# Kernel tuning notes

Hardware: AMD Instinct MI355X
Metric: run time of the kernel (lower is better)

The kernel has to match this reference:

```python
import jax, jax.numpy as jnp
import numpy as np

B, M, T, D, V = 16, 4096, 4, 256, 40000
HOPS, NLAYER, CONV_MAX = 3, 3, 512
PAD = 1  # PAD_token: embedding row zeroed (padding_idx)


def setup_inputs() -> dict:
    key = jax.random.key(0)
    ks = jax.random.split(key, 10)
    story = jax.random.randint(ks[0], (B, M, T), 0, V)
    conv_len = jax.random.randint(ks[1], (B,), 1, CONV_MAX)
    kb_len = jax.random.randint(ks[2], (B,), 0, M - CONV_MAX)
    query = jax.random.normal(ks[3], (B, 1, D), jnp.float32)
    history_outputs = jax.random.normal(ks[4], (B, CONV_MAX, D), jnp.float32)
    query_vector = jax.random.normal(ks[5], (B, D), jnp.float32)
    global_pointer = jax.random.uniform(ks[6], (B, M), jnp.float32)
    # hop+1 embedding tables, N(0, 0.1), padding row zeroed
    C_emb = jax.random.normal(ks[7], (HOPS + 1, V, D), jnp.float32) * 0.1
    C_emb = C_emb.at[:, PAD, :].set(0.0)
    Tg_w = jax.random.normal(ks[8], (HOPS + 1, D, D), jnp.float32) * 0.05
    Tg_b = jnp.zeros((HOPS + 1, D), jnp.float32)
    FW_w = jax.random.normal(ks[9], (D, D), jnp.float32) * 0.05
    FW_b = jnp.zeros((D,), jnp.float32)
    return dict(story=story, kb_len=kb_len, conv_len=conv_len, query=query,
                history_outputs=history_outputs, query_vector=query_vector,
                global_pointer=global_pointer, C_emb=C_emb, Tg_w=Tg_w,
                Tg_b=Tg_b, FW_w=FW_w, FW_b=FW_b)


def _add_lm(mem, kb_len, conv_len, hist):
    # mem: [B,M,D]; add hist[b, 0:conv_len[b]] into mem[b, kb_len[b]:kb_len[b]+conv_len[b]]
    j = jnp.arange(mem.shape[1])[None, :]                       # [1,M]
    start = kb_len[:, None]
    mask = (j >= start) & (j < start + conv_len[:, None])       # [B,M]
    idx = jnp.clip(j - start, 0, hist.shape[1] - 1)             # [B,M]
    gathered = jnp.take_along_axis(hist, idx[..., None], axis=1)  # [B,M,D]
    return mem + jnp.where(mask[..., None], gathered, 0.0)


def _embed(table, story, kb_len, conv_len, hist):
    # bag-of-words over the mem-token axis, then LM-embedding add
    e = jnp.sum(table[story], axis=2)                           # [B,M,D]
    return _add_lm(e, kb_len, conv_len, hist)


def reference(story, kb_len, conv_len, query, history_outputs, query_vector,
              global_pointer, C_emb, Tg_w, Tg_b, FW_w, FW_b):
    # ---- load_memory (eval mode: dropout is identity; ablationH/G = False) ----
    q = query[:, 0, :]                                          # [B,D]
    last_u = None
    m_story = None
    for layer in range(NLAYER):
        iq = q
        if layer > 0:
            g = jax.nn.sigmoid(iq @ Tg_w[0].T + Tg_b[0])
            iq = last_u[0] * g + iq * (1.0 - g)
        u = [iq]
        m_story = []
        embC = None
        for hop in range(HOPS):
            embA = _embed(C_emb[hop], story, kb_len, conv_len, history_outputs)
            logit = jnp.einsum('bmd,bd->bm', embA, u[-1])
            prob = jax.nn.softmax(logit, axis=1)
            embC = _embed(C_emb[hop + 1], story, kb_len, conv_len, history_outputs)
            o_k = jnp.einsum('bm,bmd->bd', prob, embC)
            u_k = u[-1] + o_k
            if layer > 0:
                g = jax.nn.sigmoid(u_k @ Tg_w[hop + 1].T + Tg_b[hop + 1])
                u_k = last_u[hop + 1] * g + u_k * (1.0 - g)
            u.append(u_k)
            m_story.append(embA)
        m_story.append(embC)
        last_u = u
        q = jax.nn.relu(u[-1] @ FW_w.T + FW_b)
    # ---- forward (decoder-side read over last layer's memories) ----
    uf = query_vector
    psoft = None
    logits = None
    for hop in range(HOPS):
        mA = m_story[hop] * global_pointer[:, :, None]
        logits = jnp.einsum('bmd,bd->bm', mA, uf)
        psoft = jax.nn.softmax(logits, axis=1)
        mC = m_story[hop + 1] * global_pointer[:, :, None]
        uf = uf + jnp.einsum('bm,bmd->bd', psoft, mC)
    return (psoft, logits, uf, m_story[-1])
```

## Files before the change

### kernel.cpp

```cpp
#include <hip/hip_runtime.h>
#include <math.h>

#define Bdim 16
#define Mdim 4096
#define Tdim 4
#define Ddim 256
#define Vdim 40000
#define CONVMAX 512

typedef float f32x4 __attribute__((ext_vector_type(4)));
static __device__ inline void nt_store4(float* p, float4 v) {
    f32x4 x = {v.x, v.y, v.z, v.w};
    __builtin_nontemporal_store(x, (f32x4*)p);
}

__global__ void init_kernel(const float* __restrict__ qv, float* __restrict__ uf) {
    int b = blockIdx.x, i = threadIdx.x;
    uf[(size_t)b * Ddim + i] = qv[(size_t)b * Ddim + i];
}

#define DOT_VT 64
#define DOT_TBLOCKS (Vdim / DOT_VT)
#define DOT_KC 64
#define HD_JPB 32
#define HD_BLOCKS (Bdim * (CONVMAX / HD_JPB))
__global__ void dot_kernel(const float* __restrict__ tab, const float* __restrict__ uf,
                           const float* __restrict__ hist,
                           float* __restrict__ D, float* __restrict__ Hdot) {
    int bid = blockIdx.x, tid = threadIdx.x;
    if (bid < DOT_TBLOCKS) {
        __shared__ __align__(16) float tl[DOT_VT][DOT_KC + 4];
        __shared__ __align__(16) float ufl[Bdim][DOT_KC + 4];
        int v0 = bid * DOT_VT;
        int vl = tid >> 3;
        int bl = tid & 7;
        int vA = vl * 2, vB = vA + 1;
        int b0 = bl * 2, b1 = b0 + 1;
        float aA0 = 0.f, aA1 = 0.f, aB0 = 0.f, aB1 = 0.f;
        for (int kc = 0; kc < Ddim; kc += DOT_KC) {
            __syncthreads();
#pragma unroll
            for (int i = 0; i < 4; ++i) {
                int idx = tid + i * 256;
                int r = idx >> 4, c4 = idx & 15;
                *(float4*)(&tl[r][c4 * 4]) =
                    *(const float4*)(tab + (size_t)(v0 + r) * Ddim + kc + c4 * 4);
            }
            {
                int r = tid >> 4, c4 = tid & 15;
                *(float4*)(&ufl[r][c4 * 4]) =
                    *(const float4*)(uf + (size_t)r * Ddim + kc + c4 * 4);
            }
            __syncthreads();
#pragma unroll
            for (int k4 = 0; k4 < DOT_KC / 4; ++k4) {
                const float4 a  = *(const float4*)(&tl[vA][k4 * 4]);
                const float4 c  = *(const float4*)(&tl[vB][k4 * 4]);
                const float4 u0 = *(const float4*)(&ufl[b0][k4 * 4]);
                const float4 u1 = *(const float4*)(&ufl[b1][k4 * 4]);
                aA0 += a.x * u0.x + a.y * u0.y + a.z * u0.z + a.w * u0.w;
                aA1 += a.x * u1.x + a.y * u1.y + a.z * u1.z + a.w * u1.w;
                aB0 += c.x * u0.x + c.y * u0.y + c.z * u0.z + c.w * u0.w;
                aB1 += c.x * u1.x + c.y * u1.y + c.z * u1.z + c.w * u1.w;
            }
        }
        size_t base = (size_t)(v0 + vA) * Bdim;
        D[base + b0] = aA0;  D[base + b1] = aA1;
        D[base + Bdim + b0] = aB0;  D[base + Bdim + b1] = aB1;
    } else {
        int r = bid - DOT_TBLOCKS;
        int b = r >> 4, j0 = (r & 15) * HD_JPB;
        int wave = tid >> 6, lane = tid & 63;
        const float4 u = *(const float4*)(uf + (size_t)b * Ddim + lane * 4);
        for (int j = j0 + wave; j < j0 + HD_JPB; j += 4) {
            const float4 h = *(const float4*)(hist + ((size_t)b * CONVMAX + j) * Ddim + lane * 4);
            float s = h.x * u.x + h.y * u.y + h.z * u.z + h.w * u.w;
#pragma unroll
            for (int off = 32; off > 0; off >>= 1) s += __shfl_xor(s, off, 64);
            if (lane == 0) Hdot[b * CONVMAX + j] = s;
        }
    }
}

__global__ void logit_kernel(const int* __restrict__ story, const int* __restrict__ kb_len,
                             const int* __restrict__ conv_len, const float* __restrict__ D,
                             const float* __restrict__ Hdot, const float* __restrict__ gp,
                             float* __restrict__ logits) {
    int row = blockIdx.x * 256 + threadIdx.x;
    int b = row >> 12, m = row & (Mdim - 1);
    const int4 st = *(const int4*)(story + (size_t)row * Tdim);
    float l = D[st.x * Bdim + b] + D[st.y * Bdim + b] + D[st.z * Bdim + b] + D[st.w * Bdim + b];
    unsigned j = (unsigned)(m - kb_len[b]);
    if (j < (unsigned)conv_len[b]) l += Hdot[b * CONVMAX + j];
    logits[row] = l * gp[row];
}

#define ZW_BLOCKS (Vdim * Bdim / 1024)
#define PW_BLOCKS (Bdim * CONVMAX / 1024)
__global__ void stats_zero_kernel(const float* __restrict__ logits, float* __restrict__ maxv,
                                  float* __restrict__ rsum, float* __restrict__ w,
                                  float* __restrict__ pwin) {
    int bid = blockIdx.x, tid = threadIdx.x;
    if (bid >= Bdim) {
        int r = bid - Bdim;
        if (r < ZW_BLOCKS) {
            *(float4*)(w + r * 1024 + tid * 4) = make_float4(0.f, 0.f, 0.f, 0.f);
        } else {
            *(float4*)(pwin + (r - ZW_BLOCKS) * 1024 + tid * 4) = make_float4(0.f, 0.f, 0.f, 0.f);
        }
        return;
    }
    __shared__ float sh[256];
    const float* lg = logits + (size_t)bid * Mdim;
    float mx = -INFINITY;
    for (int i = tid; i < Mdim; i += 256) mx = fmaxf(mx, lg[i]);
    sh[tid] = mx; __syncthreads();
    for (int s = 128; s > 0; s >>= 1) { if (tid < s) sh[tid] = fmaxf(sh[tid], sh[tid + s]); __syncthreads(); }
    float bm = sh[0]; __syncthreads();
    float sm = 0.f;
    for (int i = tid; i < Mdim; i += 256) sm += expf(lg[i] - bm);
    sh[tid] = sm; __syncthreads();
    for (int s = 128; s > 0; s >>= 1) { if (tid < s) sh[tid] += sh[tid + s]; __syncthreads(); }
    if (tid == 0) { maxv[bid] = bm; rsum[bid] = 1.0f / sh[0]; }
}

__global__ void scatter_kernel(const int* __restrict__ story, const int* __restrict__ kb_len,
                               const int* __restrict__ conv_len, const float* __restrict__ logits,
                               const float* __restrict__ maxv, const float* __restrict__ rsum,
                               const float* __restrict__ gp, float* __restrict__ w,
                               float* __restrict__ pwin) {
    int row = blockIdx.x * 256 + threadIdx.x;
    int b = row >> 12, m = row & (Mdim - 1);
    float p = expf(logits[row] - maxv[b]) * rsum[b] * gp[row];
    const int4 st = *(const int4*)(story + (size_t)row * Tdim);
    atomicAdd(&w[st.x * Bdim + b], p);
    atomicAdd(&w[st.y * Bdim + b], p);
    atomicAdd(&w[st.z * Bdim + b], p);
    atomicAdd(&w[st.w * Bdim + b], p);
    unsigned j = (unsigned)(m - kb_len[b]);
    if (j < (unsigned)conv_len[b]) pwin[b * CONVMAX + j] = p;
}

#define WS_VT 80
#define WS_TBLOCKS (Vdim / WS_VT)
#define WH_JPB 64
#define WH_BLOCKS (Bdim * (CONVMAX / WH_JPB))
__global__ void wsum_kernel(const float* __restrict__ tab, const float* __restrict__ w,
                            const float* __restrict__ pwin, const float* __restrict__ hist,
                            float* __restrict__ partial, float* __restrict__ histpart) {
    int bid = blockIdx.x, tid = threadIdx.x;
    if (bid < WS_TBLOCKS) {
        __shared__ float ws[WS_VT][Bdim];
        int v0 = bid * WS_VT;
        for (int i = tid; i < WS_VT * Bdim; i += 256) ((float*)ws)[i] = w[(size_t)v0 * Bdim + i];
        __syncthreads();
        int wave = tid >> 6, lane = tid & 63;
        int b0 = wave * 4, d4 = lane * 4;
        float4 a0 = make_float4(0.f,0.f,0.f,0.f), a1 = a0, a2 = a0, a3 = a0;
        for (int v = 0; v < WS_VT; ++v) {
            const float4 t = *(const float4*)(tab + (size_t)(v0 + v) * Ddim + d4);
            float w0 = ws[v][b0], w1 = ws[v][b0+1], w2 = ws[v][b0+2], w3 = ws[v][b0+3];
            a0.x += w0*t.x; a0.y += w0*t.y; a0.z += w0*t.z; a0.w += w0*t.w;
            a1.x += w1*t.x; a1.y += w1*t.y; a1.z += w1*t.z; a1.w += w1*t.w;
            a2.x += w2*t.x; a2.y += w2*t.y; a2.z += w2*t.z; a2.w += w2*t.w;
            a3.x += w3*t.x; a3.y += w3*t.y; a3.z += w3*t.z; a3.w += w3*t.w;
        }
        float* dst = partial + ((size_t)bid * Bdim + b0) * Ddim + d4;
        *(float4*)(dst)            = a0;
        *(float4*)(dst + Ddim)     = a1;
        *(float4*)(dst + 2 * Ddim) = a2;
        *(float4*)(dst + 3 * Ddim) = a3;
    } else {
        int r = bid - WS_TBLOCKS;
        int b = r >> 3, j0 = (r & 7) * WH_JPB;
        __shared__ float sp[WH_JPB];
        if (tid < WH_JPB) sp[tid] = pwin[b * CONVMAX + j0 + tid];
        __syncthreads();
        float acc = 0.f;
        const float* hb = hist + ((size_t)b * CONVMAX + j0) * Ddim + tid;
#pragma unroll 8
        for (int j = 0; j < WH_JPB; ++j) acc += sp[j] * hb[(size_t)j * Ddim];
        histpart[(size_t)r * Ddim + tid] = acc;
    }
}

__global__ void ufred_kernel(const float* __restrict__ partial, const float* __restrict__ histpart,
                             float* __restrict__ uf) {
    int b = blockIdx.x, tid = threadIdx.x;
    int wave = tid >> 6, lane = tid & 63, d4 = lane * 4;
    float4 acc = make_float4(0.f, 0.f, 0.f, 0.f);
    for (int s = wave; s < WS_TBLOCKS; s += 4) {
        const float4 p = *(const float4*)(partial + ((size_t)s * Bdim + b) * Ddim + d4);
        acc.x += p.x; acc.y += p.y; acc.z += p.z; acc.w += p.w;
    }
    if (wave == 0) {
#pragma unroll
        for (int c = 0; c < 8; ++c) {
            const float4 h = *(const float4*)(histpart + ((size_t)(b * 8 + c)) * Ddim + d4);
            acc.x += h.x; acc.y += h.y; acc.z += h.z; acc.w += h.w;
        }
    }
    __shared__ float4 red[4][64];
    red[wave][lane] = acc;
    __syncthreads();
    if (wave == 0) {
        float4 r0 = red[0][lane], r1 = red[1][lane], r2 = red[2][lane], r3 = red[3][lane];
        float* dst = uf + (size_t)b * Ddim + d4;
        float4 cur = *(const float4*)dst;
        cur.x += r0.x + r1.x + r2.x + r3.x;
        cur.y += r0.y + r1.y + r2.y + r3.y;
        cur.z += r0.z + r1.z + r2.z + r3.z;
        cur.w += r0.w + r1.w + r2.w + r3.w;
        *(float4*)dst = cur;
    }
}

#define MT 32
#define ATT_CH (Mdim / MT)
__global__ void att_kernel(const int* __restrict__ story, const int* __restrict__ kb_len,
                           const int* __restrict__ conv_len, const float* __restrict__ hist,
                           const float* __restrict__ tab, const float* __restrict__ logits,
                           const float* __restrict__ maxv, const float* __restrict__ rsum,
                           const float* __restrict__ gp,
                           float* __restrict__ attpart, float* __restrict__ out_m,
                           float* __restrict__ out_psoft) {
    int bid = blockIdx.x;
    int b  = bid / ATT_CH;
    int m0 = (bid % ATT_CH) * MT;
    int tid = threadIdx.x, wave = tid >> 6, lane = tid & 63;
    int d4 = lane * 4;
    __shared__ float prob[MT];
    __shared__ float4 red[4][64];
    if (tid < MT) {
        size_t row = (size_t)b * Mdim + m0 + tid;
        float pn = expf(logits[row] - maxv[b]) * rsum[b];
        __builtin_nontemporal_store(pn, out_psoft + row);
        prob[tid] = pn * gp[row];
    }
    __syncthreads();
    int kb = kb_len[b], cl = conv_len[b];
    float4 acc = make_float4(0.f, 0.f, 0.f, 0.f);
#pragma unroll 4
    for (int mm = wave; mm < MT; mm += 4) {
        int m = m0 + mm;
        size_t row = (size_t)b * Mdim + m;
        const int* st = story + row * Tdim;
        float4 v = make_float4(0.f, 0.f, 0.f, 0.f);
#pragma unroll
        for (int t = 0; t < Tdim; ++t) {
            const float4 wv = *(const float4*)(tab + (size_t)st[t] * Ddim + d4);
            v.x += wv.x; v.y += wv.y; v.z += wv.z; v.w += wv.w;
        }
        if (m >= kb && m < kb + cl) {
            const float4 h = *(const float4*)(hist + ((size_t)b * CONVMAX + (m - kb)) * Ddim + d4);
            v.x += h.x; v.y += h.y; v.z += h.z; v.w += h.w;
        }
        nt_store4(out_m + row * Ddim + d4, v);
        float p = prob[mm];
        acc.x += p * v.x; acc.y += p * v.y; acc.z += p * v.z; acc.w += p * v.w;
    }
    red[wave][lane] = acc;
    __syncthreads();
    if (wave == 0) {
        float4 a0 = red[0][lane], a1 = red[1][lane], a2 = red[2][lane], a3 = red[3][lane];
        float4 t;
        t.x = a0.x + a1.x + a2.x + a3.x;
        t.y = a0.y + a1.y + a2.y + a3.y;
        t.z = a0.z + a1.z + a2.z + a3.z;
        t.w = a0.w + a1.w + a2.w + a3.w;
        *(float4*)(attpart + (size_t)bid * Ddim + d4) = t;
    }
}

__global__ void attred_kernel(const float* __restrict__ attpart, float* __restrict__ uf) {
    int b = blockIdx.x, tid = threadIdx.x;
    int wave = tid >> 6, lane = tid & 63, d4 = lane * 4;
    float4 acc = make_float4(0.f, 0.f, 0.f, 0.f);
    for (int c = wave; c < ATT_CH; c += 4) {
        const float4 p = *(const float4*)(attpart + ((size_t)(b * ATT_CH + c)) * Ddim + d4);
        acc.x += p.x; acc.y += p.y; acc.z += p.z; acc.w += p.w;
    }
    __shared__ float4 red[4][64];
    red[wave][lane] = acc;
    __syncthreads();
    if (wave == 0) {
        float4 r0 = red[0][lane], r1 = red[1][lane], r2 = red[2][lane], r3 = red[3][lane];
        float* dst = uf + (size_t)b * Ddim + d4;
        float4 cur = *(const float4*)dst;
        cur.x += r0.x + r1.x + r2.x + r3.x;
        cur.y += r0.y + r1.y + r2.y + r3.y;
        cur.z += r0.z + r1.z + r2.z + r3.z;
        cur.w += r0.w + r1.w + r2.w + r3.w;
        *(float4*)dst = cur;
    }
}

extern "C" void kernel_launch(void* const* d_in, const int* in_sizes, int n_in,
                              void* d_out, int out_size, void* d_ws, size_t ws_size,
                              hipStream_t stream) {
    const int*   story        = (const int*)d_in[0];
    const int*   kb_len       = (const int*)d_in[1];
    const int*   conv_len     = (const int*)d_in[2];
    const float* hist         = (const float*)d_in[4];
    const float* query_vector = (const float*)d_in[5];
    const float* gp           = (const float*)d_in[6];
    const float* C_emb        = (const float*)d_in[7];

    float* out        = (float*)d_out;
    float* out_psoft  = out;
    float* out_logits = out + (size_t)Bdim * Mdim;
    float* out_uf     = out + 2 * (size_t)Bdim * Mdim;
    float* out_m      = out + 2 * (size_t)Bdim * Mdim + (size_t)Bdim * Ddim;

    float* ws = (float*)d_ws;
    float* D        = ws;
    float* w        = D + (size_t)Vdim * Bdim;
    float* Hdot     = w + (size_t)Vdim * Bdim;
    float* pwin     = Hdot + Bdim * CONVMAX;
    float* logits   = pwin + Bdim * CONVMAX;
    float* maxv     = logits + (size_t)Bdim * Mdim;
    float* rsum     = maxv + Bdim;
    float* partial  = rsum + Bdim;
    float* histpart = partial + (size_t)WS_TBLOCKS * Bdim * Ddim;
    float* attpart  = histpart + (size_t)WH_BLOCKS * Ddim;

    const size_t TAB = (size_t)Vdim * Ddim;
    const float* tab0 = C_emb;
    const float* tab1 = C_emb + TAB;
    const float* tab2 = C_emb + 2 * TAB;
    const float* tab3 = C_emb + 3 * TAB;

    const int ROW_GRID = Bdim * Mdim / 256;
    const int DOT_GRID = DOT_TBLOCKS + HD_BLOCKS;
    const int SZ_GRID  = Bdim + ZW_BLOCKS + PW_BLOCKS;
    const int WS_GRID  = WS_TBLOCKS + WH_BLOCKS;
    const int ATT_GRID = Bdim * ATT_CH;

    init_kernel<<<Bdim, Ddim, 0, stream>>>(query_vector, out_uf);

    const float* qtab[2] = { tab0, tab1 };
    const float* vtab[2] = { tab1, tab2 };
    for (int h = 0; h < 2; ++h) {
        dot_kernel<<<DOT_GRID, 256, 0, stream>>>(qtab[h], out_uf, hist, D, Hdot);
        logit_kernel<<<ROW_GRID, 256, 0, stream>>>(story, kb_len, conv_len, D, Hdot, gp, logits);
        stats_zero_kernel<<<SZ_GRID, 256, 0, stream>>>(logits, maxv, rsum, w, pwin);
        scatter_kernel<<<ROW_GRID, 256, 0, stream>>>(story, kb_len, conv_len, logits,
                                                     maxv, rsum, gp, w, pwin);
        wsum_kernel<<<WS_GRID, 256, 0, stream>>>(vtab[h], w, pwin, hist, partial, histpart);
        ufred_kernel<<<Bdim, 256, 0, stream>>>(partial, histpart, out_uf);
    }

    dot_kernel<<<DOT_GRID, 256, 0, stream>>>(tab2, out_uf, hist, D, Hdot);
    logit_kernel<<<ROW_GRID, 256, 0, stream>>>(story, kb_len, conv_len, D, Hdot, gp, out_logits);
    stats_zero_kernel<<<Bdim, 256, 0, stream>>>(out_logits, maxv, rsum, w, pwin);
    att_kernel<<<ATT_GRID, 256, 0, stream>>>(story, kb_len, conv_len, hist, tab3,
                                             out_logits, maxv, rsum, gp,
                                             attpart, out_m, out_psoft);
    attred_kernel<<<Bdim, 256, 0, stream>>>(attpart, out_uf);
}
```

Before: 493.9 us.

## Fuse logit and per-block softmax stats, split reductions with atomics

Computes the logits together with per-block max and sum inside one kernel, and has the consumers combine the 16 block stats per batch. This removes the separate stats pass that re-read the logits. The partial-sum layout becomes batch-major, and the ufred and attred reductions are split across more blocks that finish with atomicAdd into uf. WS_VT drops from 80 to 50 and the att unroll from 4 to 2. Atomic accumulation makes the floating-point summation order nondeterministic.

Result: faster. 419.4 us (-15.1%).

```diff
diff --git a/kernel.cpp b/kernel.cpp
--- a/kernel.cpp
+++ b/kernel.cpp
@@ -8,34 +8,61 @@
 #define Vdim 40000
 #define CONVMAX 512
 
+#define DOT_VT 64
+#define DOT_TILES (Vdim / DOT_VT)
+#define DOT_KC 64
+#define HD_JPB 32
+#define HD_TILES (Bdim * (CONVMAX / HD_JPB))
+#define LG_TILES (Bdim * Mdim / 256)
+#define ZW_BLOCKS (Vdim * Bdim / 1024)
+#define PW_BLOCKS (Bdim * CONVMAX / 1024)
+#define WS_VT 50
+#define WS_TILES (Vdim / WS_VT)
+#define WH_JPB 64
+#define WH_TILES (Bdim * (CONVMAX / WH_JPB))
+#define UF_CH 8
+#define UF_PER (WS_TILES / UF_CH)
+#define MT 32
+#define ATT_CH (Mdim / MT)
+#define ATT_TILES (Bdim * ATT_CH)
+
 typedef float f32x4 __attribute__((ext_vector_type(4)));
 static __device__ inline void nt_store4(float* p, float4 v) {
     f32x4 x = {v.x, v.y, v.z, v.w};
     __builtin_nontemporal_store(x, (f32x4*)p);
 }
+static __device__ inline void nt_store1(float* p, float v) {
+    __builtin_nontemporal_store(v, p);
+}
+
+static __device__ inline void combine_stats(const float* __restrict__ blockmax,
+                                            const float* __restrict__ blocksum,
+                                            int b, float* M_out, float* rs_out) {
+    float M = -INFINITY;
+#pragma unroll
+    for (int jj = 0; jj < 16; ++jj) M = fmaxf(M, blockmax[b * 16 + jj]);
+    float S = 0.f;
+#pragma unroll
+    for (int jj = 0; jj < 16; ++jj) S += blocksum[b * 16 + jj] * expf(blockmax[b * 16 + jj] - M);
+    *M_out = M;
+    *rs_out = 1.0f / S;
+}
 
 __global__ void init_kernel(const float* __restrict__ qv, float* __restrict__ uf) {
     int b = blockIdx.x, i = threadIdx.x;
     uf[(size_t)b * Ddim + i] = qv[(size_t)b * Ddim + i];
 }
 
-#define DOT_VT 64
-#define DOT_TBLOCKS (Vdim / DOT_VT)
-#define DOT_KC 64
-#define HD_JPB 32
-#define HD_BLOCKS (Bdim * (CONVMAX / HD_JPB))
 __global__ void dot_kernel(const float* __restrict__ tab, const float* __restrict__ uf,
                            const float* __restrict__ hist,
                            float* __restrict__ D, float* __restrict__ Hdot) {
     int bid = blockIdx.x, tid = threadIdx.x;
-    if (bid < DOT_TBLOCKS) {
+    if (bid < DOT_TILES) {
         __shared__ __align__(16) float tl[DOT_VT][DOT_KC + 4];
         __shared__ __align__(16) float ufl[Bdim][DOT_KC + 4];
         int v0 = bid * DOT_VT;
-        int vl = tid >> 3;
-        int bl = tid & 7;
-        int vA = vl * 2, vB = vA + 1;
-        int b0 = bl * 2, b1 = b0 + 1;
+        int vA = (tid >> 3) * 2, vB = vA + 1;
+        int bA = (tid & 7) * 2,  bB = bA + 1;
         float aA0 = 0.f, aA1 = 0.f, aB0 = 0.f, aB1 = 0.f;
         for (int kc = 0; kc < Ddim; kc += DOT_KC) {
             __syncthreads();
@@ -56,25 +83,25 @@
             for (int k4 = 0; k4 < DOT_KC / 4; ++k4) {
                 const float4 a  = *(const float4*)(&tl[vA][k4 * 4]);
                 const float4 c  = *(const float4*)(&tl[vB][k4 * 4]);
-                const float4 u0 = *(const float4*)(&ufl[b0][k4 * 4]);
-                const float4 u1 = *(const float4*)(&ufl[b1][k4 * 4]);
-                aA0 += a.x * u0.x + a.y * u0.y + a.z * u0.z + a.w * u0.w;
-                aA1 += a.x * u1.x + a.y * u1.y + a.z * u1.z + a.w * u1.w;
-                aB0 += c.x * u0.x + c.y * u0.y + c.z * u0.z + c.w * u0.w;
-                aB1 += c.x * u1.x + c.y * u1.y + c.z * u1.z + c.w * u1.w;
+                const float4 u0 = *(const float4*)(&ufl[bA][k4 * 4]);
+                const float4 u1 = *(const float4*)(&ufl[bB][k4 * 4]);
+                aA0 += a.x*u0.x + a.y*u0.y + a.z*u0.z + a.w*u0.w;
+                aA1 += a.x*u1.x + a.y*u1.y + a.z*u1.z + a.w*u1.w;
+                aB0 += c.x*u0.x + c.y*u0.y + c.z*u0.z + c.w*u0.w;
+                aB1 += c.x*u1.x + c.y*u1.y + c.z*u1.z + c.w*u1.w;
             }
         }
         size_t base = (size_t)(v0 + vA) * Bdim;
-        D[base + b0] = aA0;  D[base + b1] = aA1;
-        D[base + Bdim + b0] = aB0;  D[base + Bdim + b1] = aB1;
+        D[base + bA] = aA0;  D[base + bB] = aA1;
+        D[base + Bdim + bA] = aB0;  D[base + Bdim + bB] = aB1;
     } else {
-        int r = bid - DOT_TBLOCKS;
+        int r = bid - DOT_TILES;
         int b = r >> 4, j0 = (r & 15) * HD_JPB;
         int wave = tid >> 6, lane = tid & 63;
         const float4 u = *(const float4*)(uf + (size_t)b * Ddim + lane * 4);
         for (int j = j0 + wave; j < j0 + HD_JPB; j += 4) {
             const float4 h = *(const float4*)(hist + ((size_t)b * CONVMAX + j) * Ddim + lane * 4);
-            float s = h.x * u.x + h.y * u.y + h.z * u.z + h.w * u.w;
+            float s = h.x*u.x + h.y*u.y + h.z*u.z + h.w*u.w;
 #pragma unroll
             for (int off = 32; off > 0; off >>= 1) s += __shfl_xor(s, off, 64);
             if (lane == 0) Hdot[b * CONVMAX + j] = s;
@@ -82,56 +109,51 @@
     }
 }
 
-__global__ void logit_kernel(const int* __restrict__ story, const int* __restrict__ kb_len,
-                             const int* __restrict__ conv_len, const float* __restrict__ D,
-                             const float* __restrict__ Hdot, const float* __restrict__ gp,
-                             float* __restrict__ logits) {
-    int row = blockIdx.x * 256 + threadIdx.x;
+__global__ void logit_stats_kernel(const int* __restrict__ story, const int* __restrict__ kb_len,
+                                   const int* __restrict__ conv_len, const float* __restrict__ D,
+                                   const float* __restrict__ Hdot, const float* __restrict__ gp,
+                                   float* __restrict__ lgbuf, float* __restrict__ blockmax,
+                                   float* __restrict__ blocksum, float* __restrict__ w,
+                                   float* __restrict__ pwin) {
+    int bid = blockIdx.x, tid = threadIdx.x;
+    if (bid >= LG_TILES) {
+        int r = bid - LG_TILES;
+        if (r < ZW_BLOCKS) {
+            *(float4*)(w + (size_t)r * 1024 + tid * 4) = make_float4(0.f, 0.f, 0.f, 0.f);
+        } else {
+            *(float4*)(pwin + (size_t)(r - ZW_BLOCKS) * 1024 + tid * 4) = make_float4(0.f, 0.f, 0.f, 0.f);
+        }
+        return;
+    }
+    int row = bid * 256 + tid;
     int b = row >> 12, m = row & (Mdim - 1);
     const int4 st = *(const int4*)(story + (size_t)row * Tdim);
-    float l = D[st.x * Bdim + b] + D[st.y * Bdim + b] + D[st.z * Bdim + b] + D[st.w * Bdim + b];
+    float l = D[st.x*Bdim + b] + D[st.y*Bdim + b] + D[st.z*Bdim + b] + D[st.w*Bdim + b];
     unsigned j = (unsigned)(m - kb_len[b]);
     if (j < (unsigned)conv_len[b]) l += Hdot[b * CONVMAX + j];
-    logits[row] = l * gp[row];
-}
-
-#define ZW_BLOCKS (Vdim * Bdim / 1024)
-#define PW_BLOCKS (Bdim * CONVMAX / 1024)
-__global__ void stats_zero_kernel(const float* __restrict__ logits, float* __restrict__ maxv,
-                                  float* __restrict__ rsum, float* __restrict__ w,
-                                  float* __restrict__ pwin) {
-    int bid = blockIdx.x, tid = threadIdx.x;
-    if (bid >= Bdim) {
-        int r = bid - Bdim;
-        if (r < ZW_BLOCKS) {
-            *(float4*)(w + r * 1024 + tid * 4) = make_float4(0.f, 0.f, 0.f, 0.f);
-        } else {
-            *(float4*)(pwin + (r - ZW_BLOCKS) * 1024 + tid * 4) = make_float4(0.f, 0.f, 0.f, 0.f);
-        }
-        return;
-    }
+    l *= gp[row];
+    lgbuf[row] = l;
     __shared__ float sh[256];
-    const float* lg = logits + (size_t)bid * Mdim;
-    float mx = -INFINITY;
-    for (int i = tid; i < Mdim; i += 256) mx = fmaxf(mx, lg[i]);
-    sh[tid] = mx; __syncthreads();
+    sh[tid] = l; __syncthreads();
     for (int s = 128; s > 0; s >>= 1) { if (tid < s) sh[tid] = fmaxf(sh[tid], sh[tid + s]); __syncthreads(); }
     float bm = sh[0]; __syncthreads();
-    float sm = 0.f;
-    for (int i = tid; i < Mdim; i += 256) sm += expf(lg[i] - bm);
-    sh[tid] = sm; __syncthreads();
+    sh[tid] = expf(l - bm); __syncthreads();
     for (int s = 128; s > 0; s >>= 1) { if (tid < s) sh[tid] += sh[tid + s]; __syncthreads(); }
-    if (tid == 0) { maxv[bid] = bm; rsum[bid] = 1.0f / sh[0]; }
+    if (tid == 0) { blockmax[bid] = bm; blocksum[bid] = sh[0]; }
 }
 
 __global__ void scatter_kernel(const int* __restrict__ story, const int* __restrict__ kb_len,
                                const int* __restrict__ conv_len, const float* __restrict__ logits,
-                               const float* __restrict__ maxv, const float* __restrict__ rsum,
+                               const float* __restrict__ blockmax, const float* __restrict__ blocksum,
                                const float* __restrict__ gp, float* __restrict__ w,
                                float* __restrict__ pwin) {
-    int row = blockIdx.x * 256 + threadIdx.x;
-    int b = row >> 12, m = row & (Mdim - 1);
-    float p = expf(logits[row] - maxv[b]) * rsum[b] * gp[row];
+    int bid = blockIdx.x, tid = threadIdx.x;
+    int b = bid >> 4;
+    float M, rs;
+    combine_stats(blockmax, blocksum, b, &M, &rs);
+    int row = bid * 256 + tid;
+    int m = row & (Mdim - 1);
+    float p = expf(logits[row] - M) * rs * gp[row];
     const int4 st = *(const int4*)(story + (size_t)row * Tdim);
     atomicAdd(&w[st.x * Bdim + b], p);
     atomicAdd(&w[st.y * Bdim + b], p);
@@ -141,38 +163,34 @@
     if (j < (unsigned)conv_len[b]) pwin[b * CONVMAX + j] = p;
 }
 
-#define WS_VT 80
-#define WS_TBLOCKS (Vdim / WS_VT)
-#define WH_JPB 64
-#define WH_BLOCKS (Bdim * (CONVMAX / WH_JPB))
 __global__ void wsum_kernel(const float* __restrict__ tab, const float* __restrict__ w,
                             const float* __restrict__ pwin, const float* __restrict__ hist,
                             float* __restrict__ partial, float* __restrict__ histpart) {
     int bid = blockIdx.x, tid = threadIdx.x;
-    if (bid < WS_TBLOCKS) {
-        __shared__ float ws[WS_VT][Bdim];
+    if (bid < WS_TILES) {
+        __shared__ float wsl[WS_VT * Bdim];
         int v0 = bid * WS_VT;
-        for (int i = tid; i < WS_VT * Bdim; i += 256) ((float*)ws)[i] = w[(size_t)v0 * Bdim + i];
+        for (int i = tid; i < WS_VT * Bdim; i += 256) wsl[i] = w[(size_t)v0 * Bdim + i];
         __syncthreads();
         int wave = tid >> 6, lane = tid & 63;
         int b0 = wave * 4, d4 = lane * 4;
         float4 a0 = make_float4(0.f,0.f,0.f,0.f), a1 = a0, a2 = a0, a3 = a0;
         for (int v = 0; v < WS_VT; ++v) {
             const float4 t = *(const float4*)(tab + (size_t)(v0 + v) * Ddim + d4);
-            float w0 = ws[v][b0], w1 = ws[v][b0+1], w2 = ws[v][b0+2], w3 = ws[v][b0+3];
+            float w0 = wsl[v*Bdim + b0],   w1 = wsl[v*Bdim + b0+1];
+            float w2 = wsl[v*Bdim + b0+2], w3 = wsl[v*Bdim + b0+3];
             a0.x += w0*t.x; a0.y += w0*t.y; a0.z += w0*t.z; a0.w += w0*t.w;
             a1.x += w1*t.x; a1.y += w1*t.y; a1.z += w1*t.z; a1.w += w1*t.w;
             a2.x += w2*t.x; a2.y += w2*t.y; a2.z += w2*t.z; a2.w += w2*t.w;
             a3.x += w3*t.x; a3.y += w3*t.y; a3.z += w3*t.z; a3.w += w3*t.w;
         }
-        float* dst = partial + ((size_t)bid * Bdim + b0) * Ddim + d4;
-        *(float4*)(dst)            = a0;
-        *(float4*)(dst + Ddim)     = a1;
-        *(float4*)(dst + 2 * Ddim) = a2;
-        *(float4*)(dst + 3 * Ddim) = a3;
+        *(float4*)(&partial[((size_t)(b0+0) * WS_TILES + bid) * Ddim + d4]) = a0;
+        *(float4*)(&partial[((size_t)(b0+1) * WS_TILES + bid) * Ddim + d4]) = a1;
+        *(float4*)(&partial[((size_t)(b0+2) * WS_TILES + bid) * Ddim + d4]) = a2;
+        *(float4*)(&partial[((size_t)(b0+3) * WS_TILES + bid) * Ddim + d4]) = a3;
     } else {
-        int r = bid - WS_TBLOCKS;
-        int b = r >> 3, j0 = (r & 7) * WH_JPB;
+        int r = bid - WS_TILES;
+        int b = r >> 3, c = r & 7, j0 = c * WH_JPB;
         __shared__ float sp[WH_JPB];
         if (tid < WH_JPB) sp[tid] = pwin[b * CONVMAX + j0 + tid];
         __syncthreads();
@@ -180,67 +198,48 @@
         const float* hb = hist + ((size_t)b * CONVMAX + j0) * Ddim + tid;
 #pragma unroll 8
         for (int j = 0; j < WH_JPB; ++j) acc += sp[j] * hb[(size_t)j * Ddim];
-        histpart[(size_t)r * Ddim + tid] = acc;
+        histpart[((size_t)b * UF_CH + c) * Ddim + tid] = acc;
     }
 }
 
 __global__ void ufred_kernel(const float* __restrict__ partial, const float* __restrict__ histpart,
                              float* __restrict__ uf) {
-    int b = blockIdx.x, tid = threadIdx.x;
-    int wave = tid >> 6, lane = tid & 63, d4 = lane * 4;
-    float4 acc = make_float4(0.f, 0.f, 0.f, 0.f);
-    for (int s = wave; s < WS_TBLOCKS; s += 4) {
-        const float4 p = *(const float4*)(partial + ((size_t)s * Bdim + b) * Ddim + d4);
-        acc.x += p.x; acc.y += p.y; acc.z += p.z; acc.w += p.w;
-    }
-    if (wave == 0) {
-#pragma unroll
-        for (int c = 0; c < 8; ++c) {
-            const float4 h = *(const float4*)(histpart + ((size_t)(b * 8 + c)) * Ddim + d4);
-            acc.x += h.x; acc.y += h.y; acc.z += h.z; acc.w += h.w;
-        }
-    }
-    __shared__ float4 red[4][64];
-    red[wave][lane] = acc;
-    __syncthreads();
-    if (wave == 0) {
-        float4 r0 = red[0][lane], r1 = red[1][lane], r2 = red[2][lane], r3 = red[3][lane];
-        float* dst = uf + (size_t)b * Ddim + d4;
-        float4 cur = *(const float4*)dst;
-        cur.x += r0.x + r1.x + r2.x + r3.x;
-        cur.y += r0.y + r1.y + r2.y + r3.y;
-        cur.z += r0.z + r1.z + r2.z + r3.z;
-        cur.w += r0.w + r1.w + r2.w + r3.w;
-        *(float4*)dst = cur;
-    }
-}
-
-#define MT 32
-#define ATT_CH (Mdim / MT)
+    int b = blockIdx.x >> 3, c = blockIdx.x & 7;
+    int tid = threadIdx.x;
+    float acc = 0.f;
+    const float* base = partial + ((size_t)b * WS_TILES + c * UF_PER) * Ddim + tid;
+#pragma unroll 4
+    for (int i = 0; i < UF_PER; ++i) acc += base[(size_t)i * Ddim];
+    acc += histpart[((size_t)b * UF_CH + c) * Ddim + tid];
+    atomicAdd(&uf[(size_t)b * Ddim + tid], acc);
+}
+
 __global__ void att_kernel(const int* __restrict__ story, const int* __restrict__ kb_len,
                            const int* __restrict__ conv_len, const float* __restrict__ hist,
                            const float* __restrict__ tab, const float* __restrict__ logits,
-                           const float* __restrict__ maxv, const float* __restrict__ rsum,
+                           const float* __restrict__ blockmax, const float* __restrict__ blocksum,
                            const float* __restrict__ gp,
                            float* __restrict__ attpart, float* __restrict__ out_m,
                            float* __restrict__ out_psoft) {
     int bid = blockIdx.x;
-    int b  = bid / ATT_CH;
-    int m0 = (bid % ATT_CH) * MT;
+    int b  = bid >> 7;
+    int m0 = (bid & (ATT_CH - 1)) * MT;
     int tid = threadIdx.x, wave = tid >> 6, lane = tid & 63;
     int d4 = lane * 4;
     __shared__ float prob[MT];
     __shared__ float4 red[4][64];
     if (tid < MT) {
+        float M, rs;
+        combine_stats(blockmax, blocksum, b, &M, &rs);
         size_t row = (size_t)b * Mdim + m0 + tid;
-        float pn = expf(logits[row] - maxv[b]) * rsum[b];
-        __builtin_nontemporal_store(pn, out_psoft + row);
+        float pn = expf(logits[row] - M) * rs;
+        nt_store1(out_psoft + row, pn);
         prob[tid] = pn * gp[row];
     }
     __syncthreads();
     int kb = kb_len[b], cl = conv_len[b];
     float4 acc = make_float4(0.f, 0.f, 0.f, 0.f);
-#pragma unroll 4
+#pragma unroll 2
     for (int mm = wave; mm < MT; mm += 4) {
         int m = m0 + mm;
         size_t row = (size_t)b * Mdim + m;
@@ -263,36 +262,23 @@
     __syncthreads();
     if (wave == 0) {
         float4 a0 = red[0][lane], a1 = red[1][lane], a2 = red[2][lane], a3 = red[3][lane];
-        float4 t;
-        t.x = a0.x + a1.x + a2.x + a3.x;
-        t.y = a0.y + a1.y + a2.y + a3.y;
-        t.z = a0.z + a1.z + a2.z + a3.z;
-        t.w = a0.w + a1.w + a2.w + a3.w;
-        *(float4*)(attpart + (size_t)bid * Ddim + d4) = t;
+        float4 t4;
+        t4.x = a0.x + a1.x + a2.x + a3.x;
+        t4.y = a0.y + a1.y + a2.y + a3.y;
+        t4.z = a0.z + a1.z + a2.z + a3.z;
+        t4.w = a0.w + a1.w + a2.w + a3.w;
+        *(float4*)(&attpart[((size_t)b * ATT_CH + (bid & (ATT_CH - 1))) * Ddim + d4]) = t4;
     }
 }
 
 __global__ void attred_kernel(const float* __restrict__ attpart, float* __restrict__ uf) {
-    int b = blockIdx.x, tid = threadIdx.x;
-    int wave = tid >> 6, lane = tid & 63, d4 = lane * 4;
-    float4 acc = make_float4(0.f, 0.f, 0.f, 0.f);
-    for (int c = wave; c < ATT_CH; c += 4) {
-        const float4 p = *(const float4*)(attpart + ((size_t)(b * ATT_CH + c)) * Ddim + d4);
-        acc.x += p.x; acc.y += p.y; acc.z += p.z; acc.w += p.w;
-    }
-    __shared__ float4 red[4][64];
-    red[wave][lane] = acc;
-    __syncthreads();
-    if (wave == 0) {
-        float4 r0 = red[0][lane], r1 = red[1][lane], r2 = red[2][lane], r3 = red[3][lane];
-        float* dst = uf + (size_t)b * Ddim + d4;
-        float4 cur = *(const float4*)dst;
-        cur.x += r0.x + r1.x + r2.x + r3.x;
-        cur.y += r0.y + r1.y + r2.y + r3.y;
-        cur.z += r0.z + r1.z + r2.z + r3.z;
-        cur.w += r0.w + r1.w + r2.w + r3.w;
-        *(float4*)dst = cur;
-    }
+    int b = blockIdx.x >> 2, c = blockIdx.x & 3;
+    int tid = threadIdx.x;
+    float acc = 0.f;
+    const float* base = attpart + ((size_t)b * ATT_CH + c * 32) * Ddim + tid;
+#pragma unroll 4
+    for (int i = 0; i < 32; ++i) acc += base[(size_t)i * Ddim];
+    atomicAdd(&uf[(size_t)b * Ddim + tid], acc);
 }
 
 extern "C" void kernel_launch(void* const* d_in, const int* in_sizes, int n_in,
@@ -312,49 +298,40 @@
     float* out_uf     = out + 2 * (size_t)Bdim * Mdim;
     float* out_m      = out + 2 * (size_t)Bdim * Mdim + (size_t)Bdim * Ddim;
 
-    float* ws = (float*)d_ws;
-    float* D        = ws;
+    float* wsp = (float*)d_ws;
+    float* D        = wsp;
     float* w        = D + (size_t)Vdim * Bdim;
     float* Hdot     = w + (size_t)Vdim * Bdim;
-    float* pwin     = Hdot + Bdim * CONVMAX;
-    float* logits   = pwin + Bdim * CONVMAX;
-    float* maxv     = logits + (size_t)Bdim * Mdim;
-    float* rsum     = maxv + Bdim;
-    float* partial  = rsum + Bdim;
-    float* histpart = partial + (size_t)WS_TBLOCKS * Bdim * Ddim;
-    float* attpart  = histpart + (size_t)WH_BLOCKS * Ddim;
+    float* pwin     = Hdot + (size_t)Bdim * CONVMAX;
+    float* logits   = pwin + (size_t)Bdim * CONVMAX;
+    float* blockmax = logits + (size_t)Bdim * Mdim;
+    float* blocksum = blockmax + 256;
+    float* partial  = blocksum + 256;
+    float* histpart = partial + (size_t)Bdim * WS_TILES * Ddim;
+    float* attpart  = histpart + (size_t)Bdim * UF_CH * Ddim;
 
     const size_t TAB = (size_t)Vdim * Ddim;
-    const float* tab0 = C_emb;
-    const float* tab1 = C_emb + TAB;
-    const float* tab2 = C_emb + 2 * TAB;
-    const float* tab3 = C_emb + 3 * TAB;
-
-    const int ROW_GRID = Bdim * Mdim / 256;
-    const int DOT_GRID = DOT_TBLOCKS + HD_BLOCKS;
-    const int SZ_GRID  = Bdim + ZW_BLOCKS + PW_BLOCKS;
-    const int WS_GRID  = WS_TBLOCKS + WH_BLOCKS;
-    const int ATT_GRID = Bdim * ATT_CH;
+    const float* tab[4] = { C_emb, C_emb + TAB, C_emb + 2*TAB, C_emb + 3*TAB };
 
     init_kernel<<<Bdim, Ddim, 0, stream>>>(query_vector, out_uf);
 
-    const float* qtab[2] = { tab0, tab1 };
-    const float* vtab[2] = { tab1, tab2 };
     for (int h = 0; h < 2; ++h) {
-        dot_kernel<<<DOT_GRID, 256, 0, stream>>>(qtab[h], out_uf, hist, D, Hdot);
-        logit_kernel<<<ROW_GRID, 256, 0, stream>>>(story, kb_len, conv_len, D, Hdot, gp, logits);
-        stats_zero_kernel<<<SZ_GRID, 256, 0, stream>>>(logits, maxv, rsum, w, pwin);
-        scatter_kernel<<<ROW_GRID, 256, 0, stream>>>(story, kb_len, conv_len, logits,
-                                                     maxv, rsum, gp, w, pwin);
-        wsum_kernel<<<WS_GRID, 256, 0, stream>>>(vtab[h], w, pwin, hist, partial, histpart);
-        ufred_kernel<<<Bdim, 256, 0, stream>>>(partial, histpart, out_uf);
-    }
-
-    dot_kernel<<<DOT_GRID, 256, 0, stream>>>(tab2, out_uf, hist, D, Hdot);
-    logit_kernel<<<ROW_GRID, 256, 0, stream>>>(story, kb_len, conv_len, D, Hdot, gp, out_logits);
-    stats_zero_kernel<<<Bdim, 256, 0, stream>>>(out_logits, maxv, rsum, w, pwin);
-    att_kernel<<<ATT_GRID, 256, 0, stream>>>(story, kb_len, conv_len, hist, tab3,
-                                             out_logits, maxv, rsum, gp,
-                                             attpart, out_m, out_psoft);
-    attred_kernel<<<Bdim, 256, 0, stream>>>(attpart, out_uf);
-}
+        const float* ufsrc = (h == 0) ? query_vector : out_uf;
+        dot_kernel<<<DOT_TILES + HD_TILES, 256, 0, stream>>>(tab[h], ufsrc, hist, D, Hdot);
+        logit_stats_kernel<<<LG_TILES + ZW_BLOCKS + PW_BLOCKS, 256, 0, stream>>>(
+            story, kb_len, conv_len, D, Hdot, gp, logits, blockmax, blocksum, w, pwin);
+        scatter_kernel<<<LG_TILES, 256, 0, stream>>>(story, kb_len, conv_len, logits,
+                                                     blockmax, blocksum, gp, w, pwin);
+        wsum_kernel<<<WS_TILES + WH_TILES, 256, 0, stream>>>(tab[h + 1], w, pwin, hist,
+                                                             partial, histpart);
+        ufred_kernel<<<Bdim * UF_CH, 256, 0, stream>>>(partial, histpart, out_uf);
+    }
+
+    dot_kernel<<<DOT_TILES + HD_TILES, 256, 0, stream>>>(tab[2], out_uf, hist, D, Hdot);
+    logit_stats_kernel<<<LG_TILES, 256, 0, stream>>>(
+        story, kb_len, conv_len, D, Hdot, gp, out_logits, blockmax, blocksum, nullptr, nullptr);
+    att_kernel<<<ATT_TILES, 256, 0, stream>>>(story, kb_len, conv_len, hist, tab[3],
+                                              out_logits, blockmax, blocksum, gp,
+                                              attpart, out_m, out_psoft);
+    attred_kernel<<<Bdim * 4, 256, 0, stream>>>(attpart, out_uf);
+}
```
